# Kernel optimization log

Measured on AMD Instinct MI355X. Metric: run time of the kernel, lower is better.

The kernel has to match this reference:

```python
import jax, jax.numpy as jnp
import numpy as np

DELTA = 0.1
B, U_DIM, D_DIM, H_DIM, Y_DIM = 4096, 256, 64, 8192, 256
ORDER = H_DIM // 2  # 2x2 rotation blocks


def setup_inputs() -> dict:
    key = jax.random.key(0)
    k = jax.random.split(key, 6)
    u = jax.random.normal(k[0], (B, U_DIM), jnp.float32)
    du = jax.random.normal(k[1], (B, D_DIM), jnp.float32)
    h = jax.random.normal(k[2], (1, H_DIM), jnp.float32)          # h_init state
    # torch.nn.init.uniform_ -> U[0,1); +0.05 keeps 1/omega well-conditioned
    omega = jax.random.uniform(k[3], (ORDER,), jnp.float32) + 0.05
    B_w = jax.random.normal(k[4], (H_DIM, U_DIM + D_DIM), jnp.float32) / np.sqrt(U_DIM + D_DIM)
    C_w = jax.random.normal(k[5], (Y_DIM, H_DIM), jnp.float32) / np.sqrt(H_DIM)
    return {"u": u, "du": du, "h": h, "omega": omega, "B_w": B_w, "C_w": C_w}


def reference(u, du, h, omega, B_w, C_w):
    cos_t = jnp.cos(omega * DELTA)   # [order]
    sin_t = jnp.sin(omega * DELTA)   # [order]
    # exact rotation of state pairs: h viewed as [*, order, 2]
    hp = h.reshape(-1, ORDER, 2)
    h1 = cos_t * hp[..., 0] + sin_t * hp[..., 1]
    h2 = -sin_t * hp[..., 0] + cos_t * hp[..., 1]
    rec = jnp.stack([h1, h2], axis=-1).reshape(h.shape[0], -1)    # [1, h_dim]
    # input projection u_hat = B([du, u])
    udu = jnp.concatenate([du, u], axis=1)                        # [B, d+u]
    u_hat = (udu @ B_w.T).reshape(-1, ORDER, 2)                   # [B, order, 2]
    cm1 = cos_t - 1.0
    inp1 = (sin_t * u_hat[..., 0] - cm1 * u_hat[..., 1]) / omega
    inp2 = (cm1 * u_hat[..., 0] + sin_t * u_hat[..., 1]) / omega
    inp = jnp.stack([inp1, inp2], axis=-1).reshape(udu.shape[0], -1)  # [B, h_dim]
    h_new = rec + inp                                             # broadcast [B, h_dim]
    # sigma = identity, C linear readout (no bias)
    y = h_new @ C_w.T                                             # [B, y_dim]
    return y
```

## Files before the change

### kernel.cpp

```cpp
#include <hip/hip_runtime.h>
#include <hip/hip_bf16.h>

#define BN    4096
#define U_DIM 256
#define D_DIM 64
#define H_DIM 8192
#define Y_DIM 256
#define C_DIM 320
#define DELTAF 0.1f

typedef __bf16 bf16_t;
typedef __attribute__((ext_vector_type(8))) bf16_t bf16x8;
typedef __attribute__((ext_vector_type(4))) float f32x4;

__global__ __launch_bounds__(256) void gemm_E(
    const float* __restrict__ Cw, const float* __restrict__ Bw,
    const float* __restrict__ omega, const float* __restrict__ hin,
    float* __restrict__ E, float* __restrict__ y0) {
  const int bm = blockIdx.x;
  const int bn = blockIdx.y;
  const int ks = blockIdx.z;
  const int t = threadIdx.x;
  const int wave = t >> 6, lane = t & 63;
  const int wm = wave >> 1, wn = wave & 1;
  const int l15 = lane & 15, quad = lane >> 4;

  __shared__ bf16_t lA[64][40];
  __shared__ bf16_t lB[64][40];
  __shared__ float cS[256], cC[256], cI[256];

  const int kbeg = ks * 512;

  {
    const float om = omega[ks * 256 + t];
    const float ang = om * DELTAF;
    cS[t] = __sinf(ang);
    cC[t] = __cosf(ang) - 1.0f;
    cI[t] = 1.0f / om;
  }

  const int sr = t >> 2;
  const int sk = (t & 3) * 8;

  const float* gA = Cw + (size_t)(bm * 64 + sr) * H_DIM + sk;
  const float* gBbase = Bw + (size_t)bn * 64 + sr;

  float4 va0, va1, hv0, hv1;
  float bvals[8];
  float y0acc = 0.f;

  auto gload = [&](int kk) {
    va0 = *(const float4*)(gA + kk);
    va1 = *(const float4*)(gA + kk + 4);
    const float* pb = gBbase + (size_t)(kk + sk) * C_DIM;
#pragma unroll
    for (int j = 0; j < 8; ++j) bvals[j] = pb[(size_t)j * C_DIM];
    if (bn == 0) {
      hv0 = *(const float4*)(hin + kk + sk);
      hv1 = *(const float4*)(hin + kk + sk + 4);
    }
  };
  auto stage = [&](int i) {
    const int jp = i * 16 + (sk >> 1);
    const float4 cs = *(const float4*)&cS[jp];
    const float4 cc = *(const float4*)&cC[jp];
    const float4 ci = *(const float4*)&cI[jp];
    union {
      bf16_t h[8];
      int4 v;
    } pa, pb;
    pa.h[0] = (bf16_t)((va0.x * cs.x + va0.y * cc.x) * ci.x);
    pa.h[1] = (bf16_t)((va0.y * cs.x - va0.x * cc.x) * ci.x);
    pa.h[2] = (bf16_t)((va0.z * cs.y + va0.w * cc.y) * ci.y);
    pa.h[3] = (bf16_t)((va0.w * cs.y - va0.z * cc.y) * ci.y);
    pa.h[4] = (bf16_t)((va1.x * cs.z + va1.y * cc.z) * ci.z);
    pa.h[5] = (bf16_t)((va1.y * cs.z - va1.x * cc.z) * ci.z);
    pa.h[6] = (bf16_t)((va1.z * cs.w + va1.w * cc.w) * ci.w);
    pa.h[7] = (bf16_t)((va1.w * cs.w - va1.z * cc.w) * ci.w);
#pragma unroll
    for (int j = 0; j < 8; ++j) pb.h[j] = (bf16_t)bvals[j];
    *(int4*)&lA[sr][sk] = pa.v;
    *(int4*)&lB[sr][sk] = pb.v;
    if (bn == 0) {
      const float c0 = cc.x + 1.f, c1 = cc.y + 1.f;
      const float c2 = cc.z + 1.f, c3 = cc.w + 1.f;
      y0acc += va0.x * (c0 * hv0.x + cs.x * hv0.y) +
               va0.y * (c0 * hv0.y - cs.x * hv0.x) +
               va0.z * (c1 * hv0.z + cs.y * hv0.w) +
               va0.w * (c1 * hv0.w - cs.y * hv0.z) +
               va1.x * (c2 * hv1.x + cs.z * hv1.y) +
               va1.y * (c2 * hv1.y - cs.z * hv1.x) +
               va1.z * (c3 * hv1.z + cs.w * hv1.w) +
               va1.w * (c3 * hv1.w - cs.w * hv1.z);
    }
  };

  f32x4 acc[2][2] = {};
  gload(kbeg);
#pragma unroll
  for (int i = 0; i < 16; ++i) {
    __syncthreads();
    stage(i);
    if (i < 15) gload(kbeg + (i + 1) * 32);
    __syncthreads();
    const bf16x8 a0 = *(bf16x8*)&lA[wm * 32 + l15][quad * 8];
    const bf16x8 a1 = *(bf16x8*)&lA[wm * 32 + 16 + l15][quad * 8];
    const bf16x8 b0 = *(bf16x8*)&lB[wn * 32 + l15][quad * 8];
    const bf16x8 b1 = *(bf16x8*)&lB[wn * 32 + 16 + l15][quad * 8];
    acc[0][0] = __builtin_amdgcn_mfma_f32_16x16x32_bf16(a0, b0, acc[0][0], 0, 0, 0);
    acc[0][1] = __builtin_amdgcn_mfma_f32_16x16x32_bf16(a0, b1, acc[0][1], 0, 0, 0);
    acc[1][0] = __builtin_amdgcn_mfma_f32_16x16x32_bf16(a1, b0, acc[1][0], 0, 0, 0);
    acc[1][1] = __builtin_amdgcn_mfma_f32_16x16x32_bf16(a1, b1, acc[1][1], 0, 0, 0);
  }
#pragma unroll
  for (int mt = 0; mt < 2; ++mt)
#pragma unroll
    for (int nt = 0; nt < 2; ++nt) {
      const int col = bn * 64 + wn * 32 + nt * 16 + l15;
#pragma unroll
      for (int r = 0; r < 4; ++r) {
        const int row = bm * 64 + wm * 32 + mt * 16 + quad * 4 + r;
        atomicAdd(&E[row * C_DIM + col], acc[mt][nt][r]);
      }
    }
  if (bn == 0) {
    y0acc += __shfl_xor(y0acc, 1);
    y0acc += __shfl_xor(y0acc, 2);
    if ((t & 3) == 0) atomicAdd(&y0[bm * 64 + sr], y0acc);
  }
}

__global__ __launch_bounds__(256) void gemm_Y(
    const float* __restrict__ u, const float* __restrict__ du,
    const float* __restrict__ E, const float* __restrict__ y0,
    float* __restrict__ out) {
  const int bm = blockIdx.x;
  const int bn = blockIdx.y;
  const int t = threadIdx.x;
  const int wave = t >> 6, lane = t & 63;
  const int wm = wave >> 1, wn = wave & 1;
  const int l15 = lane & 15, quad = lane >> 4;

  __shared__ bf16_t lA[64][40];
  __shared__ bf16_t lB[64][40];

  const int sr = t >> 2;
  const int sk = (t & 3) * 8;

  float4 v0, v1, e0, e1;
  auto gload = [&](int kk) {
    const int col = kk + sk;
    if (col < D_DIM) {
      const float* p = du + (size_t)(bm * 64 + sr) * D_DIM + col;
      v0 = *(const float4*)p;
      v1 = *(const float4*)(p + 4);
    } else {
      const float* p = u + (size_t)(bm * 64 + sr) * U_DIM + (col - D_DIM);
      v0 = *(const float4*)p;
      v1 = *(const float4*)(p + 4);
    }
    const float* pe = E + (size_t)(bn * 64 + sr) * C_DIM + col;
    e0 = *(const float4*)pe;
    e1 = *(const float4*)(pe + 4);
  };
  auto stage = [&]() {
    union {
      bf16_t h[8];
      int4 v;
    } pa, pb;
    pa.h[0] = (bf16_t)v0.x; pa.h[1] = (bf16_t)v0.y;
    pa.h[2] = (bf16_t)v0.z; pa.h[3] = (bf16_t)v0.w;
    pa.h[4] = (bf16_t)v1.x; pa.h[5] = (bf16_t)v1.y;
    pa.h[6] = (bf16_t)v1.z; pa.h[7] = (bf16_t)v1.w;
    pb.h[0] = (bf16_t)e0.x; pb.h[1] = (bf16_t)e0.y;
    pb.h[2] = (bf16_t)e0.z; pb.h[3] = (bf16_t)e0.w;
    pb.h[4] = (bf16_t)e1.x; pb.h[5] = (bf16_t)e1.y;
    pb.h[6] = (bf16_t)e1.z; pb.h[7] = (bf16_t)e1.w;
    *(int4*)&lA[sr][sk] = pa.v;
    *(int4*)&lB[sr][sk] = pb.v;
  };

  f32x4 acc[2][2] = {};
  gload(0);
#pragma unroll
  for (int i = 0; i < 10; ++i) {
    __syncthreads();
    stage();
    if (i < 9) gload((i + 1) * 32);
    __syncthreads();
    const bf16x8 a0 = *(bf16x8*)&lA[wm * 32 + l15][quad * 8];
    const bf16x8 a1 = *(bf16x8*)&lA[wm * 32 + 16 + l15][quad * 8];
    const bf16x8 b0 = *(bf16x8*)&lB[wn * 32 + l15][quad * 8];
    const bf16x8 b1 = *(bf16x8*)&lB[wn * 32 + 16 + l15][quad * 8];
    acc[0][0] = __builtin_amdgcn_mfma_f32_16x16x32_bf16(a0, b0, acc[0][0], 0, 0, 0);
    acc[0][1] = __builtin_amdgcn_mfma_f32_16x16x32_bf16(a0, b1, acc[0][1], 0, 0, 0);
    acc[1][0] = __builtin_amdgcn_mfma_f32_16x16x32_bf16(a1, b0, acc[1][0], 0, 0, 0);
    acc[1][1] = __builtin_amdgcn_mfma_f32_16x16x32_bf16(a1, b1, acc[1][1], 0, 0, 0);
  }
#pragma unroll
  for (int nt = 0; nt < 2; ++nt) {
    const int col = bn * 64 + wn * 32 + nt * 16 + l15;
    const float yc = y0[col];
#pragma unroll
    for (int mt = 0; mt < 2; ++mt) {
#pragma unroll
      for (int r = 0; r < 4; ++r) {
        const int row = bm * 64 + wm * 32 + mt * 16 + quad * 4 + r;
        out[(size_t)row * Y_DIM + col] = acc[mt][nt][r] + yc;
      }
    }
  }
}

extern "C" void kernel_launch(void* const* d_in, const int* in_sizes, int n_in,
                              void* d_out, int out_size, void* d_ws,
                              size_t ws_size, hipStream_t stream) {
  const float* u = (const float*)d_in[0];
  const float* du = (const float*)d_in[1];
  const float* hin = (const float*)d_in[2];
  const float* omega = (const float*)d_in[3];
  const float* Bw = (const float*)d_in[4];
  const float* Cw = (const float*)d_in[5];
  float* out = (float*)d_out;

  char* ws = (char*)d_ws;
  float* E = (float*)ws;
  float* y0 = (float*)(ws + 327680);

  gemm_E<<<dim3(4, 5, 16), 256, 0, stream>>>(Cw, Bw, omega, hin, E, y0);
  gemm_Y<<<dim3(BN / 64, Y_DIM / 64), 256, 0, stream>>>(u, du, E, y0, out);
}
```

Baseline: 95.58 us.

## Double-buffer LDS in both GEMMs and rebalance split-K across 256 blocks

Both GEMM kernels now use two LDS buffers, so staging of the next k-tile overlaps the MFMA on the current one and one barrier per iteration goes away. gemm_E moves from a fixed 4x5x16 grid to 256 blocks that split the 20 output tiles' K range unevenly to fill all CUs. B loads are re-mapped so each wave reads consecutive columns, which gives coalesced loads. The cost is more atomics on E, a variable-length loop, and extra LDS.

```diff
diff --git a/kernel.cpp b/kernel.cpp
--- a/kernel.cpp
+++ b/kernel.cpp
@@ -17,51 +17,57 @@
     const float* __restrict__ Cw, const float* __restrict__ Bw,
     const float* __restrict__ omega, const float* __restrict__ hin,
     float* __restrict__ E, float* __restrict__ y0) {
-  const int bm = blockIdx.x;
-  const int bn = blockIdx.y;
-  const int ks = blockIdx.z;
+  const int b = blockIdx.x;
   const int t = threadIdx.x;
   const int wave = t >> 6, lane = t & 63;
   const int wm = wave >> 1, wn = wave & 1;
   const int l15 = lane & 15, quad = lane >> 4;
 
-  __shared__ bf16_t lA[64][40];
-  __shared__ bf16_t lB[64][40];
-  __shared__ float cS[256], cC[256], cI[256];
-
-  const int kbeg = ks * 512;
-
-  {
-    const float om = omega[ks * 256 + t];
+  __shared__ bf16_t lA[2][64][40];
+  __shared__ bf16_t lB[2][64][40];
+  __shared__ __align__(16) float cS[352], cC[352], cI[352];
+
+  const int p = (b * 20) >> 8;
+  const int bs = (256 * p + 19) / 20;
+  const int P = (256 * (p + 1) + 19) / 20 - bs;
+  const int c = b - bs;
+  const int it0 = (c * 256) / P;
+  const int it1 = ((c + 1) * 256) / P;
+  const int k0 = it0 * 32, k1 = it1 * 32;
+  const int niter = it1 - it0;
+  const int bm = p / 5, bn = p % 5;
+
+  const int npairs = (k1 - k0) >> 1;
+  for (int j = t; j < npairs; j += 256) {
+    const float om = omega[(k0 >> 1) + j];
     const float ang = om * DELTAF;
-    cS[t] = __sinf(ang);
-    cC[t] = __cosf(ang) - 1.0f;
-    cI[t] = 1.0f / om;
-  }
-
-  const int sr = t >> 2;
-  const int sk = (t & 3) * 8;
-
-  const float* gA = Cw + (size_t)(bm * 64 + sr) * H_DIM + sk;
-  const float* gBbase = Bw + (size_t)bn * 64 + sr;
+    cS[j] = __sinf(ang);
+    cC[j] = __cosf(ang) - 1.0f;
+    cI[j] = 1.0f / om;
+  }
+  __syncthreads();
+
+  const int ar = t >> 2, ak = (t & 3) * 8;
+  const float* gA = Cw + (size_t)(bm * 64 + ar) * H_DIM + ak;
+  const float* gBb = Bw + (size_t)bn * 64 + lane;
 
   float4 va0, va1, hv0, hv1;
-  float bvals[8];
+  float bv[8];
   float y0acc = 0.f;
 
   auto gload = [&](int kk) {
     va0 = *(const float4*)(gA + kk);
     va1 = *(const float4*)(gA + kk + 4);
-    const float* pb = gBbase + (size_t)(kk + sk) * C_DIM;
-#pragma unroll
-    for (int j = 0; j < 8; ++j) bvals[j] = pb[(size_t)j * C_DIM];
+    const float* pb = gBb + (size_t)(kk + wave * 8) * C_DIM;
+#pragma unroll
+    for (int j = 0; j < 8; ++j) bv[j] = pb[(size_t)j * C_DIM];
     if (bn == 0) {
-      hv0 = *(const float4*)(hin + kk + sk);
-      hv1 = *(const float4*)(hin + kk + sk + 4);
-    }
-  };
-  auto stage = [&](int i) {
-    const int jp = i * 16 + (sk >> 1);
+      hv0 = *(const float4*)(hin + kk + ak);
+      hv1 = *(const float4*)(hin + kk + ak + 4);
+    }
+  };
+  auto stage = [&](int kk, int buf) {
+    const int jp = ((kk - k0) >> 1) + (ak >> 1);
     const float4 cs = *(const float4*)&cS[jp];
     const float4 cc = *(const float4*)&cC[jp];
     const float4 ci = *(const float4*)&cI[jp];
@@ -78,9 +84,9 @@
     pa.h[6] = (bf16_t)((va1.z * cs.w + va1.w * cc.w) * ci.w);
     pa.h[7] = (bf16_t)((va1.w * cs.w - va1.z * cc.w) * ci.w);
 #pragma unroll
-    for (int j = 0; j < 8; ++j) pb.h[j] = (bf16_t)bvals[j];
-    *(int4*)&lA[sr][sk] = pa.v;
-    *(int4*)&lB[sr][sk] = pb.v;
+    for (int j = 0; j < 8; ++j) pb.h[j] = (bf16_t)bv[j];
+    *(int4*)&lA[buf][ar][ak] = pa.v;
+    *(int4*)&lB[buf][lane][wave * 8] = pb.v;
     if (bn == 0) {
       const float c0 = cc.x + 1.f, c1 = cc.y + 1.f;
       const float c2 = cc.z + 1.f, c3 = cc.w + 1.f;
@@ -96,22 +102,24 @@
   };
 
   f32x4 acc[2][2] = {};
-  gload(kbeg);
-#pragma unroll
-  for (int i = 0; i < 16; ++i) {
+  gload(k0);
+  stage(k0, 0);
+#pragma unroll 2
+  for (int i = 0; i < niter; ++i) {
     __syncthreads();
-    stage(i);
-    if (i < 15) gload(kbeg + (i + 1) * 32);
-    __syncthreads();
-    const bf16x8 a0 = *(bf16x8*)&lA[wm * 32 + l15][quad * 8];
-    const bf16x8 a1 = *(bf16x8*)&lA[wm * 32 + 16 + l15][quad * 8];
-    const bf16x8 b0 = *(bf16x8*)&lB[wn * 32 + l15][quad * 8];
-    const bf16x8 b1 = *(bf16x8*)&lB[wn * 32 + 16 + l15][quad * 8];
+    const int cur = i & 1;
+    if (i + 1 < niter) gload(k0 + (i + 1) * 32);
+    const bf16x8 a0 = *(bf16x8*)&lA[cur][wm * 32 + l15][quad * 8];
+    const bf16x8 a1 = *(bf16x8*)&lA[cur][wm * 32 + 16 + l15][quad * 8];
+    const bf16x8 b0 = *(bf16x8*)&lB[cur][wn * 32 + l15][quad * 8];
+    const bf16x8 b1 = *(bf16x8*)&lB[cur][wn * 32 + 16 + l15][quad * 8];
     acc[0][0] = __builtin_amdgcn_mfma_f32_16x16x32_bf16(a0, b0, acc[0][0], 0, 0, 0);
     acc[0][1] = __builtin_amdgcn_mfma_f32_16x16x32_bf16(a0, b1, acc[0][1], 0, 0, 0);
     acc[1][0] = __builtin_amdgcn_mfma_f32_16x16x32_bf16(a1, b0, acc[1][0], 0, 0, 0);
     acc[1][1] = __builtin_amdgcn_mfma_f32_16x16x32_bf16(a1, b1, acc[1][1], 0, 0, 0);
-  }
+    if (i + 1 < niter) stage(k0 + (i + 1) * 32, cur ^ 1);
+  }
+
 #pragma unroll
   for (int mt = 0; mt < 2; ++mt)
 #pragma unroll
@@ -126,7 +134,7 @@
   if (bn == 0) {
     y0acc += __shfl_xor(y0acc, 1);
     y0acc += __shfl_xor(y0acc, 2);
-    if ((t & 3) == 0) atomicAdd(&y0[bm * 64 + sr], y0acc);
+    if ((t & 3) == 0) atomicAdd(&y0[bm * 64 + ar], y0acc);
   }
 }
 
@@ -141,29 +149,29 @@
   const int wm = wave >> 1, wn = wave & 1;
   const int l15 = lane & 15, quad = lane >> 4;
 
-  __shared__ bf16_t lA[64][40];
-  __shared__ bf16_t lB[64][40];
-
-  const int sr = t >> 2;
-  const int sk = (t & 3) * 8;
+  __shared__ bf16_t lA[2][64][40];
+  __shared__ bf16_t lB[2][64][40];
+
+  const int ar = t >> 2;
+  const int ak = (t & 3) * 8;
 
   float4 v0, v1, e0, e1;
   auto gload = [&](int kk) {
-    const int col = kk + sk;
+    const int col = kk + ak;
     if (col < D_DIM) {
-      const float* p = du + (size_t)(bm * 64 + sr) * D_DIM + col;
+      const float* p = du + (size_t)(bm * 64 + ar) * D_DIM + col;
       v0 = *(const float4*)p;
       v1 = *(const float4*)(p + 4);
     } else {
-      const float* p = u + (size_t)(bm * 64 + sr) * U_DIM + (col - D_DIM);
+      const float* p = u + (size_t)(bm * 64 + ar) * U_DIM + (col - D_DIM);
       v0 = *(const float4*)p;
       v1 = *(const float4*)(p + 4);
     }
-    const float* pe = E + (size_t)(bn * 64 + sr) * C_DIM + col;
+    const float* pe = E + (size_t)(bn * 64 + ar) * C_DIM + col;
     e0 = *(const float4*)pe;
     e1 = *(const float4*)(pe + 4);
   };
-  auto stage = [&]() {
+  auto stage = [&](int buf) {
     union {
       bf16_t h[8];
       int4 v;
@@ -176,26 +184,27 @@
     pb.h[2] = (bf16_t)e0.z; pb.h[3] = (bf16_t)e0.w;
     pb.h[4] = (bf16_t)e1.x; pb.h[5] = (bf16_t)e1.y;
     pb.h[6] = (bf16_t)e1.z; pb.h[7] = (bf16_t)e1.w;
-    *(int4*)&lA[sr][sk] = pa.v;
-    *(int4*)&lB[sr][sk] = pb.v;
+    *(int4*)&lA[buf][ar][ak] = pa.v;
+    *(int4*)&lB[buf][ar][ak] = pb.v;
   };
 
   f32x4 acc[2][2] = {};
   gload(0);
+  stage(0);
 #pragma unroll
   for (int i = 0; i < 10; ++i) {
     __syncthreads();
-    stage();
+    const int cur = i & 1;
     if (i < 9) gload((i + 1) * 32);
-    __syncthreads();
-    const bf16x8 a0 = *(bf16x8*)&lA[wm * 32 + l15][quad * 8];
-    const bf16x8 a1 = *(bf16x8*)&lA[wm * 32 + 16 + l15][quad * 8];
-    const bf16x8 b0 = *(bf16x8*)&lB[wn * 32 + l15][quad * 8];
-    const bf16x8 b1 = *(bf16x8*)&lB[wn * 32 + 16 + l15][quad * 8];
+    const bf16x8 a0 = *(bf16x8*)&lA[cur][wm * 32 + l15][quad * 8];
+    const bf16x8 a1 = *(bf16x8*)&lA[cur][wm * 32 + 16 + l15][quad * 8];
+    const bf16x8 b0 = *(bf16x8*)&lB[cur][wn * 32 + l15][quad * 8];
+    const bf16x8 b1 = *(bf16x8*)&lB[cur][wn * 32 + 16 + l15][quad * 8];
     acc[0][0] = __builtin_amdgcn_mfma_f32_16x16x32_bf16(a0, b0, acc[0][0], 0, 0, 0);
     acc[0][1] = __builtin_amdgcn_mfma_f32_16x16x32_bf16(a0, b1, acc[0][1], 0, 0, 0);
     acc[1][0] = __builtin_amdgcn_mfma_f32_16x16x32_bf16(a1, b0, acc[1][0], 0, 0, 0);
     acc[1][1] = __builtin_amdgcn_mfma_f32_16x16x32_bf16(a1, b1, acc[1][1], 0, 0, 0);
+    if (i < 9) stage(cur ^ 1);
   }
 #pragma unroll
   for (int nt = 0; nt < 2; ++nt) {
@@ -227,6 +236,6 @@
   float* E = (float*)ws;
   float* y0 = (float*)(ws + 327680);
 
-  gemm_E<<<dim3(4, 5, 16), 256, 0, stream>>>(Cw, Bw, omega, hin, E, y0);
+  gemm_E<<<256, 256, 0, stream>>>(Cw, Bw, omega, hin, E, y0);
   gemm_Y<<<dim3(BN / 64, Y_DIM / 64), 256, 0, stream>>>(u, du, E, y0, out);
 }
```

Result: slower. 97.55 us (+2.1%).
